# Kernel tuning notes

Hardware: AMD Instinct MI355X
Metric: run time of the kernel (lower is better)

Reference implementation:

```python
import jax, jax.numpy as jnp
import numpy as np

B = 2
NCLS = 19    # semantic classes for the logits heads
NLAB = 20    # raw point label values 0..19 (0 = unlabeled)
# (Z, Y, X) grids at strides 2, 4, 8 of sizes=[256,256,32]
GRIDS = {2: (16, 128, 128), 4: (8, 64, 64), 8: (4, 32, 32)}


def _lin_idx(coord, Z, Y, X):
    # coord: (N,4) int rows [b, z, y, x] -> flat cell index over B*Z*Y*X
    b, z, y, x = coord[:, 0], coord[:, 1], coord[:, 2], coord[:, 3]
    return ((b * Z + z) * Y + y) * X + x


def _bev_projection(feat, coord, Y, X):
    # Fused equivalent of torch.unique + scatter_max + spconv dense():
    # scatter_max features directly into the dense (B, Y, X) BEV grid keyed by (b,y,x).
    key = (coord[:, 0] * Y + coord[:, 2]) * X + coord[:, 3]
    C = feat.shape[1]
    dense = jax.ops.segment_max(feat, key, num_segments=B * Y * X)  # empty cells -> -inf
    dense = jnp.where(jnp.isfinite(dense), dense, jnp.zeros((), feat.dtype))
    return dense.reshape(B, Y, X, C).transpose(0, 3, 1, 2)  # (B, C, Y, X)


def _voxel_sem_target(fcoord, pcoord, plabel, Z, Y, X):
    # Majority-vote semantic label per point voxel, gathered at feature voxel coords.
    ncell = B * Z * Y * X
    pair = _lin_idx(pcoord, Z, Y, X) * NLAB + plabel  # (cell, label) key
    counts = jax.ops.segment_sum(
        jnp.ones(pcoord.shape[0], jnp.int32), pair, num_segments=ncell * NLAB
    ).reshape(ncell, NLAB)
    maj = jnp.argmax(counts, axis=1).astype(jnp.int32)   # most frequent label per cell
    occ = counts.sum(axis=1) > 0                          # cell contains any point
    fk = _lin_idx(fcoord, Z, Y, X)
    return jnp.where(occ[fk], maj[fk], 0).astype(jnp.int32)  # unmatched -> 0


def _head(x, w1, g, b, w2, b2):
    # Linear(no bias) -> BatchNorm1d(train stats) -> LeakyReLU(0.1) -> Linear
    h = x @ w1
    mu = h.mean(axis=0)
    var = h.var(axis=0)
    h = (h - mu) * jax.lax.rsqrt(var + 1e-5) * g + b
    h = jnp.where(h >= 0, h, 0.1 * h)
    return h @ w2 + b2


def _rand_coords(key, n, Z, Y, X):
    kb, kz, ky, kx = jax.random.split(key, 4)
    return jnp.stack([
        jax.random.randint(kb, (n,), 0, B, dtype=jnp.int32),
        jax.random.randint(kz, (n,), 0, Z, dtype=jnp.int32),
        jax.random.randint(ky, (n,), 0, Y, dtype=jnp.int32),
        jax.random.randint(kx, (n,), 0, X, dtype=jnp.int32),
    ], axis=1)


def setup_inputs() -> dict:
    key = jax.random.key(0)
    ks = jax.random.split(key, 32)
    M1, M2, M3, NP = 200000, 100000, 50000, 500000
    inp = {
        'proj1_vw': jax.random.normal(ks[0], (M1, 64), jnp.float32),
        'proj2_vw': jax.random.normal(ks[1], (M2, 128), jnp.float32),
        'proj3_vw': jax.random.normal(ks[2], (M3, 256), jnp.float32),
        'vw1_coord': _rand_coords(ks[3], M1, *GRIDS[2]),
        'vw2_coord': _rand_coords(ks[4], M2, *GRIDS[4]),
        'vw3_coord': _rand_coords(ks[5], M3, *GRIDS[8]),
        'idx02': _rand_coords(ks[6], NP, *GRIDS[2]),
        'idx04': _rand_coords(ks[7], NP, *GRIDS[4]),
        'idx08': _rand_coords(ks[8], NP, *GRIDS[8]),
        'pw_label': jax.random.randint(ks[9], (NP,), 0, NLAB, dtype=jnp.int32),
    }
    # learned head parameters (out2 / out4 / out8)
    def head_params(k, cin):
        k1, k2 = jax.random.split(k)
        return (jax.random.normal(k1, (cin, 64), jnp.float32) * 0.02,
                jnp.ones((64,), jnp.float32), jnp.zeros((64,), jnp.float32),
                jax.random.normal(k2, (64, NCLS), jnp.float32) * 0.02,
                jnp.zeros((NCLS,), jnp.float32))
    for tag, k, cin in (('h2', ks[10], 64), ('h4', ks[11], 128), ('h8', ks[12], 256)):
        w1, g, b, w2, b2 = head_params(k, cin)
        inp[f'{tag}_w1'], inp[f'{tag}_g'], inp[f'{tag}_b'] = w1, g, b
        inp[f'{tag}_w2'], inp[f'{tag}_b2'] = w2, b2
    return inp


def reference(proj1_vw, proj2_vw, proj3_vw, vw1_coord, vw2_coord, vw3_coord,
              idx02, idx04, idx08, pw_label,
              h2_w1, h2_g, h2_b, h2_w2, h2_b2,
              h4_w1, h4_g, h4_b, h4_w2, h4_b2,
              h8_w1, h8_g, h8_b, h8_w2, h8_b2):
    (Z2, Y2, X2), (Z4, Y4, X4), (Z8, Y8, X8) = GRIDS[2], GRIDS[4], GRIDS[8]
    bev1 = _bev_projection(proj1_vw, vw1_coord, Y2, X2)   # (B, 64, 128, 128)
    bev2 = _bev_projection(proj2_vw, vw2_coord, Y4, X4)   # (B, 128, 64, 64)
    bev3 = _bev_projection(proj3_vw, vw3_coord, Y8, X8)   # (B, 256, 32, 32)
    lbl2 = _voxel_sem_target(vw1_coord, idx02, pw_label, Z2, Y2, X2)
    lbl4 = _voxel_sem_target(vw2_coord, idx04, pw_label, Z4, Y4, X4)
    lbl8 = _voxel_sem_target(vw3_coord, idx08, pw_label, Z8, Y8, X8)
    log2 = _head(proj1_vw, h2_w1, h2_g, h2_b, h2_w2, h2_b2)
    log4 = _head(proj2_vw, h4_w1, h4_g, h4_b, h4_w2, h4_b2)
    log8 = _head(proj3_vw, h8_w1, h8_g, h8_b, h8_w2, h8_b2)
    return (bev1, bev2, bev3, log2, log4, log8, lbl2, lbl4, lbl8)
```

## Files before the change

kernel.cpp:

```cpp
#include <hip/hip_runtime.h>
#include <hip/hip_bf16.h>

typedef unsigned int u32;
typedef unsigned short u16;
typedef __attribute__((ext_vector_type(8))) short short8;
typedef __attribute__((ext_vector_type(4))) float f32x4;

#define NLAB 20

#define M_1 200000
#define C_1 64
#define Z_1 16
#define Y_1 128
#define X_1 128

#define M_2 100000
#define C_2 128
#define Z_2 8
#define Y_2 64
#define X_2 64

#define M_3 50000
#define C_3 256
#define Z_3 4
#define Y_3 32
#define X_3 32

#define O_BEV1 0
#define O_BEV2 2097152
#define O_BEV3 3145728
#define O_LOG1 3670016
#define O_LOG2 7470016
#define O_LOG3 9370016
#define O_LBL1 10320016
#define O_LBL2 10520016
#define O_LBL3 10620016

#define WB_CNT 0
#define WB_CUR 43008
#define WB_PIDX 86016
#define NCELLS 43008
#define SB1 0
#define SB2 32768
#define SB3 40960

#define WBEV_F  4194304
#define WBEV2_F 6291456
#define WBEV3_F 7340032

#define WC1_W 0
#define WC2_W 2621440
#define WC3_W 2949120
#define W_COUNT_BYTES 11960320ull
#define WH1 0
#define WH2 12800000
#define WH3 19200000
#define WPART 12000000
#define WP1 0
#define WP2 200064
#define WP3 300160
#define WSTATS 12350208

#define GB1 1563
#define GB2 782
#define GB3 391
#define HB1 782
#define HB2 391
#define HB3 196

static __device__ __forceinline__ u16 f2bf(float f) {
  u32 u = __float_as_uint(f);
  u32 r = u + 0x7fffu + ((u >> 16) & 1u);
  return (u16)(r >> 16);
}

__global__ __launch_bounds__(256) void k_cellcount(
    const int* __restrict__ co1, const int* __restrict__ co2, const int* __restrict__ co3,
    int* __restrict__ cnt)
{
  int blk = blockIdx.x;
  const int* co; int Y, X, M, base, m;
  if (blk < HB1)            { co = co1; Y = Y_1; X = X_1; M = M_1; base = SB1; m = blk * 256 + threadIdx.x; }
  else if (blk < HB1 + HB2) { co = co2; Y = Y_2; X = X_2; M = M_2; base = SB2; m = (blk - HB1) * 256 + threadIdx.x; }
  else                      { co = co3; Y = Y_3; X = X_3; M = M_3; base = SB3; m = (blk - HB1 - HB2) * 256 + threadIdx.x; }
  if (m >= M) return;
  int4 c = *(const int4*)(co + m * 4);
  atomicAdd(cnt + base + (c.x * Y + c.z) * X + c.w, 1);
}

__global__ __launch_bounds__(1024) void k_scan(const int* __restrict__ cnt, int* __restrict__ cur) {
  int t = threadIdx.x;
  int local[42];
  int s = 0;
#pragma unroll
  for (int j = 0; j < 42; j++) { local[j] = cnt[t * 42 + j]; s += local[j]; }
  __shared__ int red[1024];
  red[t] = s;
  __syncthreads();
  for (int off = 1; off < 1024; off <<= 1) {
    int v = (t >= off) ? red[t - off] : 0;
    __syncthreads();
    red[t] += v;
    __syncthreads();
  }
  int base = red[t] - s;
#pragma unroll
  for (int j = 0; j < 42; j++) { cur[t * 42 + j] = base; base += local[j]; }
}

__global__ __launch_bounds__(256) void k_scatter(
    const int* __restrict__ co1, const int* __restrict__ co2, const int* __restrict__ co3,
    int* __restrict__ cur, int* __restrict__ pidx)
{
  int blk = blockIdx.x;
  const int* co; int Y, X, M, base, m;
  if (blk < HB1)            { co = co1; Y = Y_1; X = X_1; M = M_1; base = SB1; m = blk * 256 + threadIdx.x; }
  else if (blk < HB1 + HB2) { co = co2; Y = Y_2; X = X_2; M = M_2; base = SB2; m = (blk - HB1) * 256 + threadIdx.x; }
  else                      { co = co3; Y = Y_3; X = X_3; M = M_3; base = SB3; m = (blk - HB1 - HB2) * 256 + threadIdx.x; }
  if (m >= M) return;
  int4 c = *(const int4*)(co + m * 4);
  int slot = atomicAdd(cur + base + (c.x * Y + c.z) * X + c.w, 1);
  pidx[slot] = m;
}

#define GBATCH 8
__global__ __launch_bounds__(256) void k_bevgather(
    const float* __restrict__ f1, const float* __restrict__ f2, const float* __restrict__ f3,
    const int* __restrict__ cnt, const int* __restrict__ cur,
    const int* __restrict__ pidx, float* __restrict__ ws)
{
  int wid = blockIdx.x * 4 + (threadIdx.x >> 6);
  int lane = threadIdx.x & 63;
  const float* f; int cidx; size_t wbase; int C;
  if (wid < 32768) {
    f = f1; C = 64; cidx = SB1 + wid; wbase = WBEV_F + (size_t)wid * 64;
  } else if (wid < 49152) {
    int u = wid - 32768; int cell = u >> 1, ch = (u & 1) * 64;
    f = f2 + ch; C = 128; cidx = SB2 + cell; wbase = WBEV2_F + (size_t)cell * 128 + ch;
  } else {
    int u = wid - 49152; int cell = u >> 2, ch = (u & 3) * 64;
    f = f3 + ch; C = 256; cidx = SB3 + cell; wbase = WBEV3_F + (size_t)cell * 256 + ch;
  }
  int n = cnt[cidx], end = cur[cidx];
  float acc = __uint_as_float(0xff800000u);
  for (int i = end - n; i < end; i += GBATCH) {
    int p[GBATCH];
#pragma unroll
    for (int j = 0; j < GBATCH; j++) {
      int idx = i + j;
      p[j] = pidx[idx < end ? idx : end - 1];
    }
    float v[GBATCH];
#pragma unroll
    for (int j = 0; j < GBATCH; j++) v[j] = f[(size_t)p[j] * C + lane];
#pragma unroll
    for (int j = 0; j < GBATCH; j++) acc = fmaxf(acc, v[j]);
  }
  ws[wbase + lane] = (n > 0) ? acc : 0.f;
}

__global__ __launch_bounds__(256) void k_bevt(
    const float* __restrict__ ws, float* __restrict__ out)
{
  __shared__ float tileU[4160];
  int bid = blockIdx.x, tid = threadIdx.x;
  if (bid < 512) {
    int b = bid >> 8, y = (bid >> 1) & 127, x0 = (bid & 1) * 64;
    const float* src = ws + WBEV_F + (size_t)((b * 128 + y) * 128 + x0) * 64;
#pragma unroll
    for (int pass = 0; pass < 16; pass++) {
      int idx = pass * 256 + tid;
      int x = idx >> 6, c = idx & 63;
      tileU[x * 65 + c] = src[(size_t)x * 64 + c];
    }
    __syncthreads();
    size_t ob = O_BEV1 + ((size_t)(b * 64) * 128 + y) * 128 + x0;
#pragma unroll
    for (int pass = 0; pass < 16; pass++) {
      int idx = pass * 256 + tid;
      int c = idx >> 6, x = idx & 63;
      out[ob + (size_t)c * 16384 + x] = tileU[x * 65 + c];
    }
  } else if (bid < 768) {
    int t = bid - 512;
    int b = t >> 7, y = (t >> 1) & 63, x0 = (t & 1) * 32;
    const float* src = ws + WBEV2_F + (size_t)((b * 64 + y) * 64 + x0) * 128;
#pragma unroll
    for (int pass = 0; pass < 16; pass++) {
      int idx = pass * 256 + tid;
      int x = idx >> 7, c = idx & 127;
      tileU[x * 129 + c] = src[(size_t)x * 128 + c];
    }
    __syncthreads();
    size_t ob = O_BEV2 + ((size_t)(b * 128) * 64 + y) * 64 + x0;
#pragma unroll
    for (int pass = 0; pass < 16; pass++) {
      int idx = pass * 256 + tid;
      int c = idx >> 5, x = idx & 31;
      out[ob + (size_t)c * 4096 + x] = tileU[x * 129 + c];
    }
  } else {
    int t = bid - 768;
    int b = t >> 6, y = (t >> 1) & 31, ch0 = (t & 1) * 128;
    const float* src = ws + WBEV3_F + (size_t)((b * 32 + y) * 32) * 256 + ch0;
#pragma unroll
    for (int pass = 0; pass < 16; pass++) {
      int idx = pass * 256 + tid;
      int x = idx >> 7, c = idx & 127;
      tileU[x * 129 + c] = src[(size_t)x * 256 + c];
    }
    __syncthreads();
    size_t ob = O_BEV3 + ((size_t)(b * 256 + ch0) * 32 + y) * 32;
#pragma unroll
    for (int pass = 0; pass < 16; pass++) {
      int idx = pass * 256 + tid;
      int c = idx >> 5, x = idx & 31;
      out[ob + (size_t)c * 1024 + x] = tileU[x * 129 + c];
    }
  }
}

__global__ __launch_bounds__(256) void k_count(
    const int* __restrict__ i2, const int* __restrict__ i4, const int* __restrict__ i8,
    const int* __restrict__ lab, u32* __restrict__ cnt)
{
  int blk = blockIdx.x;
  const int* pc; int Z, Y, X; u32* base; int i;
  if (blk < 1954)      { pc = i2; Z = Z_1; Y = Y_1; X = X_1; base = cnt + WC1_W; i = blk * 256 + threadIdx.x; }
  else if (blk < 3908) { pc = i4; Z = Z_2; Y = Y_2; X = X_2; base = cnt + WC2_W; i = (blk - 1954) * 256 + threadIdx.x; }
  else                 { pc = i8; Z = Z_3; Y = Y_3; X = X_3; base = cnt + WC3_W; i = (blk - 3908) * 256 + threadIdx.x; }
  if (i >= 500000) return;
  int4 c = *(const int4*)(pc + i * 4);
  int l = lab[i];
  int lin = ((c.x * Z + c.y) * Y + c.z) * X + c.w;
  atomicAdd(base + lin * 5 + (l >> 2), 1u << ((l & 3) * 8));
}

__global__ __launch_bounds__(256) void k_lbl(
    const int* __restrict__ fc1, const int* __restrict__ fc2, const int* __restrict__ fc3,
    const u32* __restrict__ cnt, float* __restrict__ out)
{
  int blk = blockIdx.x;
  const int* fc; int Z, Y, X, M; const u32* base; long lbase; int m;
  if (blk < HB1)            { fc = fc1; Z = Z_1; Y = Y_1; X = X_1; M = M_1; base = cnt + WC1_W; lbase = O_LBL1; m = blk * 256 + threadIdx.x; }
  else if (blk < HB1 + HB2) { fc = fc2; Z = Z_2; Y = Y_2; X = X_2; M = M_2; base = cnt + WC2_W; lbase = O_LBL2; m = (blk - HB1) * 256 + threadIdx.x; }
  else                      { fc = fc3; Z = Z_3; Y = Y_3; X = X_3; M = M_3; base = cnt + WC3_W; lbase = O_LBL3; m = (blk - HB1 - HB2) * 256 + threadIdx.x; }
  if (m >= M) return;
  int4 c = *(const int4*)(fc + m * 4);
  int lin = ((c.x * Z + c.y) * Y + c.z) * X + c.w;
  const u32* cp = base + lin * 5;
  u32 w0 = cp[0], w1 = cp[1], w2 = cp[2], w3 = cp[3], w4 = cp[4];
  int best = (int)(w0 & 0xffu); int bi = 0;
#pragma unroll
  for (int n = 1; n < NLAB; n++) {
    u32 w = (n < 4) ? w0 : (n < 8) ? w1 : (n < 12) ? w2 : (n < 16) ? w3 : w4;
    int cc = (int)((w >> ((n & 3) * 8)) & 0xffu);
    if (cc > best) { best = cc; bi = n; }
  }
  out[lbase + m] = (float)bi;
}

__global__ __launch_bounds__(256) void k_gemm(
    const float* __restrict__ x1, const float* __restrict__ x2, const float* __restrict__ x3,
    const float* __restrict__ w1a, const float* __restrict__ w1b, const float* __restrict__ w1c,
    u16* __restrict__ hbuf, float* __restrict__ part)
{
  int blk = blockIdx.x;
  const float* x; const float* w1; u16* h; float* pp; int Cin, M, bl, NB;
  if (blk < GB1)            { x = x1; w1 = w1a; h = hbuf + WH1; pp = part + WP1; Cin = C_1; M = M_1; bl = blk;             NB = GB1; }
  else if (blk < GB1 + GB2) { x = x2; w1 = w1b; h = hbuf + WH2; pp = part + WP2; Cin = C_2; M = M_2; bl = blk - GB1;       NB = GB2; }
  else                      { x = x3; w1 = w1c; h = hbuf + WH3; pp = part + WP3; Cin = C_3; M = M_3; bl = blk - GB1 - GB2; NB = GB3; }
  int tid = threadIdx.x;
  int lane = tid & 63, wv = tid >> 6;
  int m16 = lane & 15, quad = lane >> 4;

  __shared__ u16 As[128 * 72];
  __shared__ u16 Bs[64 * 72];
  __shared__ float redS[4][64];
  __shared__ float redQ[4][64];

  f32x4 acc[2][4];
#pragma unroll
  for (int mt = 0; mt < 2; mt++)
#pragma unroll
    for (int nt = 0; nt < 4; nt++) acc[mt][nt] = (f32x4){0.f, 0.f, 0.f, 0.f};

  int nchunk = Cin >> 6;
  for (int c = 0; c < nchunk; c++) {
    if (c) __syncthreads();
#pragma unroll
    for (int pass = 0; pass < 8; pass++) {
      int fidx = pass * 256 + tid;
      int row = fidx >> 4, kp = (fidx & 15) * 4;
      int grow = bl * 128 + row;
      float4 v = make_float4(0.f, 0.f, 0.f, 0.f);
      if (grow < M) v = *(const float4*)(x + (size_t)grow * Cin + c * 64 + kp);
      ushort4 o = { f2bf(v.x), f2bf(v.y), f2bf(v.z), f2bf(v.w) };
      *(ushort4*)(As + row * 72 + kp) = o;
    }
    {
      int n = tid & 63, kg = tid >> 6;
#pragma unroll
      for (int p = 0; p < 4; p++) {
        int k0 = kg * 4 + p * 16;
        const float* wp = w1 + (size_t)(c * 64 + k0) * 64 + n;
        ushort4 o = { f2bf(wp[0]), f2bf(wp[64]), f2bf(wp[128]), f2bf(wp[192]) };
        *(ushort4*)(Bs + n * 72 + k0) = o;
      }
    }
    __syncthreads();
#pragma unroll
    for (int ks = 0; ks < 2; ks++) {
      short8 a0 = *(const short8*)(As + (wv * 32 + m16) * 72 + ks * 32 + quad * 8);
      short8 a1 = *(const short8*)(As + (wv * 32 + 16 + m16) * 72 + ks * 32 + quad * 8);
      short8 b[4];
#pragma unroll
      for (int nt = 0; nt < 4; nt++)
        b[nt] = *(const short8*)(Bs + (nt * 16 + m16) * 72 + ks * 32 + quad * 8);
#pragma unroll
      for (int nt = 0; nt < 4; nt++) {
        acc[0][nt] = __builtin_amdgcn_mfma_f32_16x16x32_bf16(a0, b[nt], acc[0][nt], 0, 0, 0);
        acc[1][nt] = __builtin_amdgcn_mfma_f32_16x16x32_bf16(a1, b[nt], acc[1][nt], 0, 0, 0);
      }
    }
  }

  float s[4] = {0.f, 0.f, 0.f, 0.f}, q[4] = {0.f, 0.f, 0.f, 0.f};
#pragma unroll
  for (int mt = 0; mt < 2; mt++) {
#pragma unroll
    for (int nt = 0; nt < 4; nt++) {
#pragma unroll
      for (int r = 0; r < 4; r++) {
        float v = acc[mt][nt][r];
        int grow = bl * 128 + wv * 32 + mt * 16 + quad * 4 + r;
        if (grow < M) h[(size_t)grow * 64 + nt * 16 + m16] = f2bf(v);
        s[nt] += v;
        q[nt] = fmaf(v, v, q[nt]);
      }
    }
  }
#pragma unroll
  for (int nt = 0; nt < 4; nt++) {
    s[nt] += __shfl_xor(s[nt], 16); s[nt] += __shfl_xor(s[nt], 32);
    q[nt] += __shfl_xor(q[nt], 16); q[nt] += __shfl_xor(q[nt], 32);
  }
  if (lane < 16) {
#pragma unroll
    for (int nt = 0; nt < 4; nt++) {
      redS[wv][nt * 16 + lane] = s[nt];
      redQ[wv][nt * 16 + lane] = q[nt];
    }
  }
  __syncthreads();
  if (tid < 64) {
    pp[tid * NB + bl] = redS[0][tid] + redS[1][tid] + redS[2][tid] + redS[3][tid];
  } else if (tid < 128) {
    int n2 = tid - 64;
    pp[(64 + n2) * NB + bl] = redQ[0][n2] + redQ[1][n2] + redQ[2][n2] + redQ[3][n2];
  }
}

__global__ __launch_bounds__(256) void k_stats(const float* __restrict__ part, float* __restrict__ stats,
    const float* __restrict__ g1, const float* __restrict__ b1,
    const float* __restrict__ g4, const float* __restrict__ b4,
    const float* __restrict__ g8, const float* __restrict__ b8)
{
  int blk = blockIdx.x;
  int sc = blk >> 6, col = blk & 63;
  int nb; const float* p; float invM; const float* g; const float* bb;
  if (sc == 0)      { nb = GB1; p = part + WP1; invM = 1.f / M_1; g = g1; bb = b1; }
  else if (sc == 1) { nb = GB2; p = part + WP2; invM = 1.f / M_2; g = g4; bb = b4; }
  else              { nb = GB3; p = part + WP3; invM = 1.f / M_3; g = g8; bb = b8; }
  int t = threadIdx.x;
  const float* ps = p + (size_t)col * nb;
  const float* pq = p + (size_t)(64 + col) * nb;
  float s = 0.f, q = 0.f;
  for (int i = t; i < nb; i += 256) { s += ps[i]; q += pq[i]; }
  __shared__ float r1[256], r2[256];
  r1[t] = s; r2[t] = q;
  __syncthreads();
  for (int off = 128; off > 0; off >>= 1) {
    if (t < off) { r1[t] += r1[t + off]; r2[t] += r2[t + off]; }
    __syncthreads();
  }
  if (t == 0) {
    float mu  = r1[0] * invM;
    float var = r2[0] * invM - mu * mu;
    float scale = rsqrtf(var + 1e-5f) * g[col];
    stats[sc * 128 + col]      = scale;
    stats[sc * 128 + 64 + col] = fmaf(-mu, scale, bb[col]);
  }
}

__global__ __launch_bounds__(256) void k_head(
    const u16* __restrict__ hbuf, const float* __restrict__ stats,
    const float* __restrict__ w21, const float* __restrict__ c21,
    const float* __restrict__ w24, const float* __restrict__ c24,
    const float* __restrict__ w28, const float* __restrict__ c28,
    float* __restrict__ out)
{
  int blk = blockIdx.x;
  const u16* h; const float* st; const float* w2; const float* b2;
  int M; long obase; int bl;
  if (blk < HB1)            { h = hbuf + WH1; st = stats;       w2 = w21; b2 = c21; M = M_1; obase = O_LOG1; bl = blk; }
  else if (blk < HB1 + HB2) { h = hbuf + WH2; st = stats + 128; w2 = w24; b2 = c24; M = M_2; obase = O_LOG2; bl = blk - HB1; }
  else                      { h = hbuf + WH3; st = stats + 256; w2 = w28; b2 = c28; M = M_3; obase = O_LOG3; bl = blk - HB1 - HB2; }
  int tid = threadIdx.x;
  int rowbase = bl * 256;
  int avail = M - rowbase; if (avail > 256) avail = 256;

  __shared__ __align__(16) float os[256 * 19];

  float acc[19];
#pragma unroll
  for (int n = 0; n < 19; n++) acc[n] = 0.f;

  if (tid < avail) {
    const uint4* hr = (const uint4*)(h + (size_t)(rowbase + tid) * 64);
    uint4 d[8];
#pragma unroll
    for (int q = 0; q < 8; q++) d[q] = hr[q];
#pragma unroll
    for (int q = 0; q < 8; q++) {
#pragma unroll
      for (int half = 0; half < 2; half++) {
        u32 dx = half ? d[q].z : d[q].x;
        u32 dy = half ? d[q].w : d[q].y;
        int j = q * 8 + half * 4;
        float f0 = __uint_as_float(dx << 16);
        float f1 = __uint_as_float(dx & 0xffff0000u);
        float f2 = __uint_as_float(dy << 16);
        float f3 = __uint_as_float(dy & 0xffff0000u);
        float a0 = fmaf(f0, st[j],     st[64 + j]);     a0 = a0 >= 0.f ? a0 : 0.1f * a0;
        float a1 = fmaf(f1, st[j + 1], st[64 + j + 1]); a1 = a1 >= 0.f ? a1 : 0.1f * a1;
        float a2 = fmaf(f2, st[j + 2], st[64 + j + 2]); a2 = a2 >= 0.f ? a2 : 0.1f * a2;
        float a3 = fmaf(f3, st[j + 3], st[64 + j + 3]); a3 = a3 >= 0.f ? a3 : 0.1f * a3;
#pragma unroll
        for (int n = 0; n < 19; n++) {
          acc[n] = fmaf(a0, w2[j * 19 + n], acc[n]);
          acc[n] = fmaf(a1, w2[(j + 1) * 19 + n], acc[n]);
          acc[n] = fmaf(a2, w2[(j + 2) * 19 + n], acc[n]);
          acc[n] = fmaf(a3, w2[(j + 3) * 19 + n], acc[n]);
        }
      }
    }
#pragma unroll
    for (int n = 0; n < 19; n++) os[tid * 19 + n] = acc[n] + b2[n];
  }
  __syncthreads();
  int tot = avail * 19;
  float* op = out + obase + (size_t)rowbase * 19;
  for (int i = tid; i < tot; i += 256) op[i] = os[i];
}

extern "C" void kernel_launch(void* const* d_in, const int* in_sizes, int n_in,
                              void* d_out, int out_size, void* d_ws, size_t ws_size,
                              hipStream_t stream) {
  (void)in_sizes; (void)n_in; (void)out_size; (void)ws_size;
  const float* p1 = (const float*)d_in[0];
  const float* p2 = (const float*)d_in[1];
  const float* p3 = (const float*)d_in[2];
  const int* vc1  = (const int*)d_in[3];
  const int* vc2  = (const int*)d_in[4];
  const int* vc3  = (const int*)d_in[5];
  const int* i2   = (const int*)d_in[6];
  const int* i4   = (const int*)d_in[7];
  const int* i8   = (const int*)d_in[8];
  const int* lab  = (const int*)d_in[9];
  const float* h2w1 = (const float*)d_in[10]; const float* h2g = (const float*)d_in[11];
  const float* h2b  = (const float*)d_in[12]; const float* h2w2 = (const float*)d_in[13];
  const float* h2b2 = (const float*)d_in[14];
  const float* h4w1 = (const float*)d_in[15]; const float* h4g = (const float*)d_in[16];
  const float* h4b  = (const float*)d_in[17]; const float* h4w2 = (const float*)d_in[18];
  const float* h4b2 = (const float*)d_in[19];
  const float* h8w1 = (const float*)d_in[20]; const float* h8g = (const float*)d_in[21];
  const float* h8b  = (const float*)d_in[22]; const float* h8w2 = (const float*)d_in[23];
  const float* h8b2 = (const float*)d_in[24];

  float* out = (float*)d_out;
  int* wsi = (int*)d_ws;
  u32* wsu = (u32*)d_ws;
  float* wsf = (float*)d_ws;
  u16* wsh = (u16*)d_ws;

  hipMemsetAsync(wsi + WB_CNT, 0, NCELLS * sizeof(int), stream);
  k_cellcount<<<HB1 + HB2 + HB3, 256, 0, stream>>>(vc1, vc2, vc3, wsi + WB_CNT);
  k_scan<<<1, 1024, 0, stream>>>(wsi + WB_CNT, wsi + WB_CUR);
  k_scatter<<<HB1 + HB2 + HB3, 256, 0, stream>>>(vc1, vc2, vc3, wsi + WB_CUR, wsi + WB_PIDX);
  k_bevgather<<<14336, 256, 0, stream>>>(p1, p2, p3, wsi + WB_CNT, wsi + WB_CUR, wsi + WB_PIDX, wsf);
  k_bevt<<<896, 256, 0, stream>>>(wsf, out);

  hipMemsetAsync(d_ws, 0, W_COUNT_BYTES, stream);
  k_count<<<5862, 256, 0, stream>>>(i2, i4, i8, lab, wsu);
  k_lbl<<<HB1 + HB2 + HB3, 256, 0, stream>>>(vc1, vc2, vc3, wsu, out);

  k_gemm<<<GB1 + GB2 + GB3, 256, 0, stream>>>(p1, p2, p3, h2w1, h4w1, h8w1, wsh, wsf + WPART);
  k_stats<<<192, 256, 0, stream>>>(wsf + WPART, wsf + WSTATS, h2g, h2b, h4g, h4b, h8g, h8b);
  k_head<<<HB1 + HB2 + HB3, 256, 0, stream>>>((const u16*)d_ws, wsf + WSTATS,
      h2w2, h2b2, h4w2, h4b2, h8w2, h8b2, out);
}
```

Before: 474.9 us.

## Merge BEV gather with label histogram, and transpose with label vote

Moves the label-count histogram to its own region of the workspace so it no longer aliases the BEV scratch. That lets the histogram clear happen up front and the two independent pipelines share kernels. The BEV gather and the label atomic histogram now run as one grid, as do the BEV transpose and the majority-vote label kernel. This cuts two launches and lets independent work overlap, at the cost of more branch-heavy, heterogeneous blocks.

Measured after the change: 460.0 us. -3.1%, faster.

```diff
diff --git a/kernel.cpp b/kernel.cpp
--- a/kernel.cpp
+++ b/kernel.cpp
@@ -48,9 +48,9 @@
 #define WBEV2_F 6291456
 #define WBEV3_F 7340032
 
-#define WC1_W 0
-#define WC2_W 2621440
-#define WC3_W 2949120
+#define WC1_W 8388608
+#define WC2_W 11010048
+#define WC3_W 11337728
 #define W_COUNT_BYTES 11960320ull
 #define WH1 0
 #define WH2 12800000
@@ -124,46 +124,86 @@
 }
 
 #define GBATCH 8
-__global__ __launch_bounds__(256) void k_bevgather(
+__global__ __launch_bounds__(256) void k_gc(
     const float* __restrict__ f1, const float* __restrict__ f2, const float* __restrict__ f3,
     const int* __restrict__ cnt, const int* __restrict__ cur,
-    const int* __restrict__ pidx, float* __restrict__ ws)
-{
-  int wid = blockIdx.x * 4 + (threadIdx.x >> 6);
-  int lane = threadIdx.x & 63;
-  const float* f; int cidx; size_t wbase; int C;
-  if (wid < 32768) {
-    f = f1; C = 64; cidx = SB1 + wid; wbase = WBEV_F + (size_t)wid * 64;
-  } else if (wid < 49152) {
-    int u = wid - 32768; int cell = u >> 1, ch = (u & 1) * 64;
-    f = f2 + ch; C = 128; cidx = SB2 + cell; wbase = WBEV2_F + (size_t)cell * 128 + ch;
+    const int* __restrict__ pidx, float* __restrict__ ws,
+    const int* __restrict__ i2, const int* __restrict__ i4, const int* __restrict__ i8,
+    const int* __restrict__ lab, u32* __restrict__ hist)
+{
+  int blk = blockIdx.x;
+  if (blk < 14336) {
+    int wid = blk * 4 + (threadIdx.x >> 6);
+    int lane = threadIdx.x & 63;
+    const float* f; int cidx; size_t wbase; int C;
+    if (wid < 32768) {
+      f = f1; C = 64; cidx = SB1 + wid; wbase = WBEV_F + (size_t)wid * 64;
+    } else if (wid < 49152) {
+      int u = wid - 32768; int cell = u >> 1, ch = (u & 1) * 64;
+      f = f2 + ch; C = 128; cidx = SB2 + cell; wbase = WBEV2_F + (size_t)cell * 128 + ch;
+    } else {
+      int u = wid - 49152; int cell = u >> 2, ch = (u & 3) * 64;
+      f = f3 + ch; C = 256; cidx = SB3 + cell; wbase = WBEV3_F + (size_t)cell * 256 + ch;
+    }
+    int n = cnt[cidx], end = cur[cidx];
+    float acc = __uint_as_float(0xff800000u);
+    for (int i = end - n; i < end; i += GBATCH) {
+      int p[GBATCH];
+#pragma unroll
+      for (int j = 0; j < GBATCH; j++) {
+        int idx = i + j;
+        p[j] = pidx[idx < end ? idx : end - 1];
+      }
+      float v[GBATCH];
+#pragma unroll
+      for (int j = 0; j < GBATCH; j++) v[j] = f[(size_t)p[j] * C + lane];
+#pragma unroll
+      for (int j = 0; j < GBATCH; j++) acc = fmaxf(acc, v[j]);
+    }
+    ws[wbase + lane] = (n > 0) ? acc : 0.f;
   } else {
-    int u = wid - 49152; int cell = u >> 2, ch = (u & 3) * 64;
-    f = f3 + ch; C = 256; cidx = SB3 + cell; wbase = WBEV3_F + (size_t)cell * 256 + ch;
-  }
-  int n = cnt[cidx], end = cur[cidx];
-  float acc = __uint_as_float(0xff800000u);
-  for (int i = end - n; i < end; i += GBATCH) {
-    int p[GBATCH];
-#pragma unroll
-    for (int j = 0; j < GBATCH; j++) {
-      int idx = i + j;
-      p[j] = pidx[idx < end ? idx : end - 1];
-    }
-    float v[GBATCH];
-#pragma unroll
-    for (int j = 0; j < GBATCH; j++) v[j] = f[(size_t)p[j] * C + lane];
-#pragma unroll
-    for (int j = 0; j < GBATCH; j++) acc = fmaxf(acc, v[j]);
-  }
-  ws[wbase + lane] = (n > 0) ? acc : 0.f;
-}
-
-__global__ __launch_bounds__(256) void k_bevt(
-    const float* __restrict__ ws, float* __restrict__ out)
-{
+    int cb = blk - 14336;
+    const int* pc; int Z, Y, X; u32* base; int i;
+    if (cb < 1954)      { pc = i2; Z = Z_1; Y = Y_1; X = X_1; base = hist + WC1_W; i = cb * 256 + threadIdx.x; }
+    else if (cb < 3908) { pc = i4; Z = Z_2; Y = Y_2; X = X_2; base = hist + WC2_W; i = (cb - 1954) * 256 + threadIdx.x; }
+    else                { pc = i8; Z = Z_3; Y = Y_3; X = X_3; base = hist + WC3_W; i = (cb - 3908) * 256 + threadIdx.x; }
+    if (i >= 500000) return;
+    int4 c = *(const int4*)(pc + i * 4);
+    int l = lab[i];
+    int lin = ((c.x * Z + c.y) * Y + c.z) * X + c.w;
+    atomicAdd(base + lin * 5 + (l >> 2), 1u << ((l & 3) * 8));
+  }
+}
+
+__global__ __launch_bounds__(256) void k_tl(
+    const float* __restrict__ ws, const u32* __restrict__ hist,
+    const int* __restrict__ fc1, const int* __restrict__ fc2, const int* __restrict__ fc3,
+    float* __restrict__ out)
+{
+  int blk = blockIdx.x;
+  int tid = threadIdx.x;
+  if (blk < HB1 + HB2 + HB3) {
+    const int* fc; int Z, Y, X, M; const u32* base; long lbase; int m;
+    if (blk < HB1)            { fc = fc1; Z = Z_1; Y = Y_1; X = X_1; M = M_1; base = hist + WC1_W; lbase = O_LBL1; m = blk * 256 + tid; }
+    else if (blk < HB1 + HB2) { fc = fc2; Z = Z_2; Y = Y_2; X = X_2; M = M_2; base = hist + WC2_W; lbase = O_LBL2; m = (blk - HB1) * 256 + tid; }
+    else                      { fc = fc3; Z = Z_3; Y = Y_3; X = X_3; M = M_3; base = hist + WC3_W; lbase = O_LBL3; m = (blk - HB1 - HB2) * 256 + tid; }
+    if (m >= M) return;
+    int4 c = *(const int4*)(fc + m * 4);
+    int lin = ((c.x * Z + c.y) * Y + c.z) * X + c.w;
+    const u32* cp = base + lin * 5;
+    u32 w0 = cp[0], w1 = cp[1], w2 = cp[2], w3 = cp[3], w4 = cp[4];
+    int best = (int)(w0 & 0xffu); int bi = 0;
+#pragma unroll
+    for (int n = 1; n < NLAB; n++) {
+      u32 w = (n < 4) ? w0 : (n < 8) ? w1 : (n < 12) ? w2 : (n < 16) ? w3 : w4;
+      int cc = (int)((w >> ((n & 3) * 8)) & 0xffu);
+      if (cc > best) { best = cc; bi = n; }
+    }
+    out[lbase + m] = (float)bi;
+    return;
+  }
   __shared__ float tileU[4160];
-  int bid = blockIdx.x, tid = threadIdx.x;
+  int bid = blk - (HB1 + HB2 + HB3);
   if (bid < 512) {
     int b = bid >> 8, y = (bid >> 1) & 127, x0 = (bid & 1) * 64;
     const float* src = ws + WBEV_F + (size_t)((b * 128 + y) * 128 + x0) * 64;
@@ -218,46 +258,6 @@
       out[ob + (size_t)c * 1024 + x] = tileU[x * 129 + c];
     }
   }
-}
-
-__global__ __launch_bounds__(256) void k_count(
-    const int* __restrict__ i2, const int* __restrict__ i4, const int* __restrict__ i8,
-    const int* __restrict__ lab, u32* __restrict__ cnt)
-{
-  int blk = blockIdx.x;
-  const int* pc; int Z, Y, X; u32* base; int i;
-  if (blk < 1954)      { pc = i2; Z = Z_1; Y = Y_1; X = X_1; base = cnt + WC1_W; i = blk * 256 + threadIdx.x; }
-  else if (blk < 3908) { pc = i4; Z = Z_2; Y = Y_2; X = X_2; base = cnt + WC2_W; i = (blk - 1954) * 256 + threadIdx.x; }
-  else                 { pc = i8; Z = Z_3; Y = Y_3; X = X_3; base = cnt + WC3_W; i = (blk - 3908) * 256 + threadIdx.x; }
-  if (i >= 500000) return;
-  int4 c = *(const int4*)(pc + i * 4);
-  int l = lab[i];
-  int lin = ((c.x * Z + c.y) * Y + c.z) * X + c.w;
-  atomicAdd(base + lin * 5 + (l >> 2), 1u << ((l & 3) * 8));
-}
-
-__global__ __launch_bounds__(256) void k_lbl(
-    const int* __restrict__ fc1, const int* __restrict__ fc2, const int* __restrict__ fc3,
-    const u32* __restrict__ cnt, float* __restrict__ out)
-{
-  int blk = blockIdx.x;
-  const int* fc; int Z, Y, X, M; const u32* base; long lbase; int m;
-  if (blk < HB1)            { fc = fc1; Z = Z_1; Y = Y_1; X = X_1; M = M_1; base = cnt + WC1_W; lbase = O_LBL1; m = blk * 256 + threadIdx.x; }
-  else if (blk < HB1 + HB2) { fc = fc2; Z = Z_2; Y = Y_2; X = X_2; M = M_2; base = cnt + WC2_W; lbase = O_LBL2; m = (blk - HB1) * 256 + threadIdx.x; }
-  else                      { fc = fc3; Z = Z_3; Y = Y_3; X = X_3; M = M_3; base = cnt + WC3_W; lbase = O_LBL3; m = (blk - HB1 - HB2) * 256 + threadIdx.x; }
-  if (m >= M) return;
-  int4 c = *(const int4*)(fc + m * 4);
-  int lin = ((c.x * Z + c.y) * Y + c.z) * X + c.w;
-  const u32* cp = base + lin * 5;
-  u32 w0 = cp[0], w1 = cp[1], w2 = cp[2], w3 = cp[3], w4 = cp[4];
-  int best = (int)(w0 & 0xffu); int bi = 0;
-#pragma unroll
-  for (int n = 1; n < NLAB; n++) {
-    u32 w = (n < 4) ? w0 : (n < 8) ? w1 : (n < 12) ? w2 : (n < 16) ? w3 : w4;
-    int cc = (int)((w >> ((n & 3) * 8)) & 0xffu);
-    if (cc > best) { best = cc; bi = n; }
-  }
-  out[lbase + m] = (float)bi;
 }
 
 __global__ __launch_bounds__(256) void k_gemm(
@@ -485,15 +485,17 @@
   u16* wsh = (u16*)d_ws;
 
   hipMemsetAsync(wsi + WB_CNT, 0, NCELLS * sizeof(int), stream);
+  hipMemsetAsync(wsu + WC1_W, 0, W_COUNT_BYTES, stream);
+
   k_cellcount<<<HB1 + HB2 + HB3, 256, 0, stream>>>(vc1, vc2, vc3, wsi + WB_CNT);
   k_scan<<<1, 1024, 0, stream>>>(wsi + WB_CNT, wsi + WB_CUR);
   k_scatter<<<HB1 + HB2 + HB3, 256, 0, stream>>>(vc1, vc2, vc3, wsi + WB_CUR, wsi + WB_PIDX);
-  k_bevgather<<<14336, 256, 0, stream>>>(p1, p2, p3, wsi + WB_CNT, wsi + WB_CUR, wsi + WB_PIDX, wsf);
-  k_bevt<<<896, 256, 0, stream>>>(wsf, out);
-
-  hipMemsetAsync(d_ws, 0, W_COUNT_BYTES, stream);
-  k_count<<<5862, 256, 0, stream>>>(i2, i4, i8, lab, wsu);
-  k_lbl<<<HB1 + HB2 + HB3, 256, 0, stream>>>(vc1, vc2, vc3, wsu, out);
+
+  k_gc<<<14336 + 5862, 256, 0, stream>>>(p1, p2, p3,
+      wsi + WB_CNT, wsi + WB_CUR, wsi + WB_PIDX, wsf,
+      i2, i4, i8, lab, wsu);
+
+  k_tl<<<HB1 + HB2 + HB3 + 896, 256, 0, stream>>>(wsf, wsu, vc1, vc2, vc3, out);
 
   k_gemm<<<GB1 + GB2 + GB3, 256, 0, stream>>>(p1, p2, p3, h2w1, h4w1, h8w1, wsh, wsf + WPART);
   k_stats<<<192, 256, 0, stream>>>(wsf + WPART, wsf + WSTATS, h2g, h2b, h4g, h4b, h8g, h8b);
```
